# Performance work log

Hardware: AMD Instinct MI355X
Metric: run time of the kernel (lower is better)

## Reference

```python
import jax, jax.numpy as jnp
import numpy as np

DIM = 1024
HEADS = 16
HEAD_DIM = DIM // HEADS
SCALE = HEAD_DIM ** -0.5


def setup_inputs() -> dict:
    key = jax.random.key(0)
    k1, k2, k3 = jax.random.split(key, 3)
    x = jax.random.normal(k1, (4, 2048, DIM), dtype=jnp.float32)
    Wqkv = jax.random.normal(k2, (DIM, 3 * DIM), dtype=jnp.float32) * (DIM ** -0.5)
    Wout = jax.random.normal(k3, (DIM, DIM), dtype=jnp.float32) * (DIM ** -0.5)
    bout = jnp.zeros((DIM,), dtype=jnp.float32)
    return {"x": x, "Wqkv": Wqkv, "Wout": Wout, "bout": bout}


def reference(x, Wqkv, Wout, bout):
    b, n, _ = x.shape
    qkv = x @ Wqkv  # [b, n, 3*dim]
    q, k, v = jnp.split(qkv, 3, axis=-1)
    # [b, n, dim] -> [b, h, n, d]
    def split_heads(t):
        return t.reshape(b, n, HEADS, HEAD_DIM).transpose(0, 2, 1, 3)
    q, k, v = split_heads(q), split_heads(k), split_heads(v)
    dots = jnp.einsum('bhid,bhjd->bhij', q, k) * SCALE
    attn = jax.nn.softmax(dots, axis=-1)
    out = jnp.einsum('bhij,bhjd->bhid', attn, v)
    out = out.transpose(0, 2, 1, 3).reshape(b, n, DIM)
    return out @ Wout + bout  # dropout is identity in eval mode
```

## Files before the change

### kernel.cpp

```cpp
#include <hip/hip_runtime.h>
#include <hip/hip_bf16.h>

#define BATCH 4
#define SEQ   2048
#define DIM   1024
#define HEADS 16
#define HD    64
#define ROWS  (BATCH * SEQ)
#define QKV_N (3 * DIM)
#define ATT_C 0.18033688011f

typedef unsigned short u16;
typedef _Float16 half8 __attribute__((ext_vector_type(8)));
typedef _Float16 half4v __attribute__((ext_vector_type(4)));
typedef float f32x4 __attribute__((ext_vector_type(4)));

__device__ __forceinline__ void gload_lds16(const u16* g, u16* l) {
  typedef const __attribute__((address_space(1))) unsigned int* gp_t;
  typedef __attribute__((address_space(3))) unsigned int* lp_t;
  __builtin_amdgcn_global_load_lds((gp_t)(const void*)g, (lp_t)(void*)l, 16, 0, 0);
}

__global__ __launch_bounds__(256) void conv_x(const float* __restrict__ x,
                                              u16* __restrict__ xh) {
  int i = blockIdx.x * 256 + threadIdx.x;
  float4 v = ((const float4*)x)[i];
  half4v h = {(_Float16)v.x, (_Float16)v.y, (_Float16)v.z, (_Float16)v.w};
  *(half4v*)&xh[(size_t)i * 4] = h;
}

__global__ __launch_bounds__(256) void conv_w(const float* __restrict__ W,
                                              u16* __restrict__ Wt,
                                              int K, int N) {
  __shared__ float T[64][65];
  const int tid = threadIdx.x;
  const int k0 = blockIdx.y * 64, n0 = blockIdx.x * 64;
#pragma unroll
  for (int j = 0; j < 4; ++j) {
    int k = j * 16 + (tid >> 4), n4 = (tid & 15) * 4;
    float4 v = *(const float4*)(W + (size_t)(k0 + k) * N + n0 + n4);
    T[k][n4 + 0] = v.x; T[k][n4 + 1] = v.y; T[k][n4 + 2] = v.z; T[k][n4 + 3] = v.w;
  }
  __syncthreads();
#pragma unroll
  for (int j = 0; j < 4; ++j) {
    int n = j * 16 + (tid >> 4), k4 = (tid & 15) * 4;
    half4v w = {(_Float16)T[k4 + 0][n], (_Float16)T[k4 + 1][n],
                (_Float16)T[k4 + 2][n], (_Float16)T[k4 + 3][n]};
    *(half4v*)&Wt[(size_t)(n0 + n) * K + k0 + k4] = w;
  }
}

template <int MODE>
__global__ __launch_bounds__(256) void gemm_bt(
    const u16* __restrict__ A, const u16* __restrict__ Bt,
    const float* __restrict__ bias, void* __restrict__ Cv,
    u16* __restrict__ Qg, u16* __restrict__ Kg, u16* __restrict__ VtG,
    int M, int N, int K) {
  __shared__ u16 As[128 * 32];
  __shared__ u16 Bs[128 * 32];

  const int tid = threadIdx.x;
  const int wave = tid >> 6, lane = tid & 63;
  const int q4 = lane >> 4, c = lane & 15;
  const int wm = wave >> 1, wn = wave & 1;
  const int row0 = blockIdx.y * 128, col0 = blockIdx.x * 128;
  const int rr = lane >> 2, seg = lane & 3;

  f32x4 acc[4][4];
#pragma unroll
  for (int mi = 0; mi < 4; ++mi)
#pragma unroll
    for (int ni = 0; ni < 4; ++ni) acc[mi][ni] = (f32x4){0.f, 0.f, 0.f, 0.f};

  for (int k0 = 0; k0 < K; k0 += 32) {
#pragma unroll
    for (int i = 0; i < 2; ++i) {
      int chunk = wave * 2 + i;
      gload_lds16(A + (size_t)(row0 + chunk * 16 + rr) * K + k0 + seg * 8,
                  &As[chunk * 512]);
      gload_lds16(Bt + (size_t)(col0 + chunk * 16 + rr) * K + k0 + seg * 8,
                  &Bs[chunk * 512]);
    }
    __syncthreads();

    half8 af[4], bf[4];
#pragma unroll
    for (int mi = 0; mi < 4; ++mi)
      af[mi] = *(const half8*)&As[(wm * 64 + mi * 16 + c) * 32 + q4 * 8];
#pragma unroll
    for (int ni = 0; ni < 4; ++ni)
      bf[ni] = *(const half8*)&Bs[(wn * 64 + ni * 16 + c) * 32 + q4 * 8];
#pragma unroll
    for (int mi = 0; mi < 4; ++mi)
#pragma unroll
      for (int ni = 0; ni < 4; ++ni)
        acc[mi][ni] = __builtin_amdgcn_mfma_f32_16x16x32_f16(
            af[mi], bf[ni], acc[mi][ni], 0, 0, 0);
    __syncthreads();
  }

#pragma unroll
  for (int mi = 0; mi < 4; ++mi)
#pragma unroll
    for (int ni = 0; ni < 4; ++ni) {
      int colg = col0 + wn * 64 + ni * 16 + c;
      if (MODE == 0) {
        float bv = bias[colg];
#pragma unroll
        for (int r = 0; r < 4; ++r) {
          int rowg = row0 + wm * 64 + mi * 16 + q4 * 4 + r;
          ((float*)Cv)[(size_t)rowg * N + colg] = acc[mi][ni][r] + bv;
        }
      } else {
        int rowg0 = row0 + wm * 64 + mi * 16 + q4 * 4;
        int b  = rowg0 >> 11;
        int which = colg >> 10;
        int rem = colg & 1023;
        int hh = rem >> 6, d = rem & 63;
        size_t bh = (size_t)(b * HEADS + hh);
        if (which == 2) {
          int i0 = rowg0 & 2047;
          half4v pv = {(_Float16)acc[mi][ni][0], (_Float16)acc[mi][ni][1],
                       (_Float16)acc[mi][ni][2], (_Float16)acc[mi][ni][3]};
          *(half4v*)&VtG[(bh * HD + d) * SEQ + i0] = pv;
        } else {
          u16* dst = (which == 0) ? Qg : Kg;
          float sc = (which == 0) ? ATT_C : 1.0f;
#pragma unroll
          for (int r = 0; r < 4; ++r) {
            int i = (rowg0 + r) & 2047;
            ((_Float16*)dst)[(bh * SEQ + i) * HD + d] =
                (_Float16)(acc[mi][ni][r] * sc);
          }
        }
      }
    }
}

__global__ __launch_bounds__(256, 3) void attn_mfma(
    const u16* __restrict__ Qg, const u16* __restrict__ Kg,
    const u16* __restrict__ VtG, u16* __restrict__ ctx) {
  const int L  = blockIdx.x;
  const int bh = L & 63;
  const int b  = bh >> 4, h = bh & 15;
  const int qt = L >> 6;

  __shared__ u16 Ks[2][64 * 32];
  __shared__ u16 Vt[2][64 * 32];
  __shared__ u16 Ps[128 * 72];
  __shared__ float lred[4][128];
  __shared__ float lfull[128];

  const int tid  = threadIdx.x;
  const int wave = tid >> 6;
  const int lane = tid & 63;
  const int q4   = lane >> 4;
  const int c    = lane & 15;
  const int rr   = lane >> 2, seg = lane & 3;
  const int sseg = seg ^ (rr & 3);
  const int rsw  = (c & 3);

  const size_t bhb = (size_t)bh;
  const int qrow0 = qt * 128;

  half8 qf[8][2];
#pragma unroll
  for (int nt = 0; nt < 8; ++nt)
#pragma unroll
    for (int half = 0; half < 2; ++half)
      qf[nt][half] = *(const half8*)&Qg[(bhb * SEQ + qrow0 + nt * 16 + c) * HD
                                        + half * 32 + q4 * 8];

  f32x4 o_acc[2][4];
#pragma unroll
  for (int sub = 0; sub < 2; ++sub)
#pragma unroll
    for (int dt = 0; dt < 4; ++dt) o_acc[sub][dt] = (f32x4){0.f, 0.f, 0.f, 0.f};
  float lp[8] = {0.f, 0.f, 0.f, 0.f, 0.f, 0.f, 0.f, 0.f};

  for (int j0 = 0; j0 < SEQ; j0 += 64) {
    __syncthreads();
#pragma unroll
    for (int half = 0; half < 2; ++half) {
      gload_lds16(Kg + (bhb * SEQ + j0 + wave * 16 + rr) * HD
                      + half * 32 + sseg * 8,
                  &Ks[half][wave * 16 * 32]);
      gload_lds16(VtG + (bhb * HD + wave * 16 + rr) * SEQ + j0
                      + half * 32 + sseg * 8,
                  &Vt[half][wave * 16 * 32]);
    }
    __syncthreads();

    half8 af0 = *(const half8*)&Ks[0][(wave * 16 + c) * 32 + (q4 ^ rsw) * 8];
    half8 af1 = *(const half8*)&Ks[1][(wave * 16 + c) * 32 + (q4 ^ rsw) * 8];
#pragma unroll
    for (int nt = 0; nt < 8; ++nt) {
      f32x4 st = (f32x4){0.f, 0.f, 0.f, 0.f};
      st = __builtin_amdgcn_mfma_f32_16x16x32_f16(af0, qf[nt][0], st, 0, 0, 0);
      st = __builtin_amdgcn_mfma_f32_16x16x32_f16(af1, qf[nt][1], st, 0, 0, 0);
      float p0 = __builtin_amdgcn_exp2f(st[0]);
      float p1 = __builtin_amdgcn_exp2f(st[1]);
      float p2 = __builtin_amdgcn_exp2f(st[2]);
      float p3 = __builtin_amdgcn_exp2f(st[3]);
      lp[nt] += (p0 + p1) + (p2 + p3);
      half4v w = {(_Float16)p0, (_Float16)p1, (_Float16)p2, (_Float16)p3};
      *(half4v*)&Ps[(nt * 16 + c) * 72 + wave * 16 + q4 * 4] = w;
    }
    __syncthreads();

    half8 vb0[4], vb1[4];
#pragma unroll
    for (int dt = 0; dt < 4; ++dt) {
      vb0[dt] = *(const half8*)&Vt[0][(dt * 16 + c) * 32 + (q4 ^ rsw) * 8];
      vb1[dt] = *(const half8*)&Vt[1][(dt * 16 + c) * 32 + (q4 ^ rsw) * 8];
    }
#pragma unroll
    for (int sub = 0; sub < 2; ++sub) {
      half8 pa0 = *(const half8*)&Ps[(wave * 32 + sub * 16 + c) * 72 + q4 * 8];
      half8 pa1 = *(const half8*)&Ps[(wave * 32 + sub * 16 + c) * 72 + 32 + q4 * 8];
#pragma unroll
      for (int dt = 0; dt < 4; ++dt) {
        o_acc[sub][dt] = __builtin_amdgcn_mfma_f32_16x16x32_f16(
            pa0, vb0[dt], o_acc[sub][dt], 0, 0, 0);
        o_acc[sub][dt] = __builtin_amdgcn_mfma_f32_16x16x32_f16(
            pa1, vb1[dt], o_acc[sub][dt], 0, 0, 0);
      }
    }
  }

#pragma unroll
  for (int nt = 0; nt < 8; ++nt) {
    lp[nt] += __shfl_xor(lp[nt], 16);
    lp[nt] += __shfl_xor(lp[nt], 32);
  }
  if (q4 == 0)
#pragma unroll
    for (int nt = 0; nt < 8; ++nt) lred[wave][nt * 16 + c] = lp[nt];
  __syncthreads();
  if (tid < 128)
    lfull[tid] = lred[0][tid] + lred[1][tid] + lred[2][tid] + lred[3][tid];
  __syncthreads();

#pragma unroll
  for (int sub = 0; sub < 2; ++sub)
#pragma unroll
    for (int r = 0; r < 4; ++r) {
      int i = wave * 32 + sub * 16 + q4 * 4 + r;
      float inv = 1.0f / lfull[i];
      size_t row = (size_t)b * SEQ + qrow0 + i;
#pragma unroll
      for (int dt = 0; dt < 4; ++dt)
        ((_Float16*)ctx)[row * DIM + h * HD + dt * 16 + c] =
            (_Float16)(o_acc[sub][dt][r] * inv);
    }
}

extern "C" void kernel_launch(void* const* d_in, const int* in_sizes, int n_in,
                              void* d_out, int out_size, void* d_ws, size_t ws_size,
                              hipStream_t stream) {
  const float* x    = (const float*)d_in[0];
  const float* Wqkv = (const float*)d_in[1];
  const float* Wout = (const float*)d_in[2];
  const float* bout = (const float*)d_in[3];
  float* out = (float*)d_out;

  u16* xh   = (u16*)d_ws;
  u16* Wqt  = xh  + (size_t)ROWS * DIM;
  u16* Wot  = Wqt + (size_t)QKV_N * DIM;
  u16* Qg   = Wot + (size_t)DIM * DIM;
  u16* Kg   = Qg  + (size_t)BATCH * HEADS * SEQ * HD;
  u16* VtG  = Kg  + (size_t)BATCH * HEADS * SEQ * HD;
  u16* ctxh = VtG + (size_t)BATCH * HEADS * HD * SEQ;

  conv_x<<<ROWS * DIM / 4 / 256, 256, 0, stream>>>(x, xh);
  conv_w<<<dim3(QKV_N / 64, DIM / 64), 256, 0, stream>>>(Wqkv, Wqt, DIM, QKV_N);
  conv_w<<<dim3(DIM / 64, DIM / 64), 256, 0, stream>>>(Wout, Wot, DIM, DIM);

  gemm_bt<1><<<dim3(QKV_N / 128, ROWS / 128), 256, 0, stream>>>(
      xh, Wqt, nullptr, nullptr, Qg, Kg, VtG, ROWS, QKV_N, DIM);

  attn_mfma<<<dim3(1024), 256, 0, stream>>>(Qg, Kg, VtG, ctxh);

  gemm_bt<0><<<dim3(DIM / 128, ROWS / 128), 256, 0, stream>>>(
      ctxh, Wot, bout, out, nullptr, nullptr, nullptr, ROWS, DIM, DIM);
}
```

Baseline: 313.2 us.

## Double-buffer K/V LDS tiles in attention kernel to prefetch next block

Splits the K and V LDS tiles into two buffers. The next 64-key tile is issued via global_load_lds at the start of each iteration, while the current tile is consumed from the other buffer. This drops the leading barrier pair per iteration in favour of one trailing barrier, aiming to hide global load latency behind the QK^T and softmax work. The cost is twice the LDS for K/V. The existing mid-loop barrier may force an early wait on the outstanding loads, which would limit how much overlap is gained.

```diff
diff --git a/kernel.cpp b/kernel.cpp
--- a/kernel.cpp
+++ b/kernel.cpp
@@ -146,8 +146,8 @@
   const int b  = bh >> 4, h = bh & 15;
   const int qt = L >> 6;
 
-  __shared__ u16 Ks[2][64 * 32];
-  __shared__ u16 Vt[2][64 * 32];
+  __shared__ u16 Ks[2][2][64 * 32];
+  __shared__ u16 Vt[2][2][64 * 32];
   __shared__ u16 Ps[128 * 72];
   __shared__ float lred[4][128];
   __shared__ float lfull[128];
@@ -164,6 +164,14 @@
   const size_t bhb = (size_t)bh;
   const int qrow0 = qt * 128;
 
+#pragma unroll
+  for (int half = 0; half < 2; ++half) {
+    gload_lds16(Kg + (bhb * SEQ + wave * 16 + rr) * HD + half * 32 + sseg * 8,
+                &Ks[0][half][wave * 16 * 32]);
+    gload_lds16(VtG + (bhb * HD + wave * 16 + rr) * SEQ + half * 32 + sseg * 8,
+                &Vt[0][half][wave * 16 * 32]);
+  }
+
   half8 qf[8][2];
 #pragma unroll
   for (int nt = 0; nt < 8; ++nt)
@@ -179,21 +187,26 @@
     for (int dt = 0; dt < 4; ++dt) o_acc[sub][dt] = (f32x4){0.f, 0.f, 0.f, 0.f};
   float lp[8] = {0.f, 0.f, 0.f, 0.f, 0.f, 0.f, 0.f, 0.f};
 
+  __syncthreads();
+
   for (int j0 = 0; j0 < SEQ; j0 += 64) {
-    __syncthreads();
-#pragma unroll
-    for (int half = 0; half < 2; ++half) {
-      gload_lds16(Kg + (bhb * SEQ + j0 + wave * 16 + rr) * HD
-                      + half * 32 + sseg * 8,
-                  &Ks[half][wave * 16 * 32]);
-      gload_lds16(VtG + (bhb * HD + wave * 16 + rr) * SEQ + j0
-                      + half * 32 + sseg * 8,
-                  &Vt[half][wave * 16 * 32]);
-    }
-    __syncthreads();
-
-    half8 af0 = *(const half8*)&Ks[0][(wave * 16 + c) * 32 + (q4 ^ rsw) * 8];
-    half8 af1 = *(const half8*)&Ks[1][(wave * 16 + c) * 32 + (q4 ^ rsw) * 8];
+    const int cb = (j0 >> 6) & 1;
+
+    if (j0 + 64 < SEQ) {
+      const int jn = j0 + 64, nb = cb ^ 1;
+#pragma unroll
+      for (int half = 0; half < 2; ++half) {
+        gload_lds16(Kg + (bhb * SEQ + jn + wave * 16 + rr) * HD
+                        + half * 32 + sseg * 8,
+                    &Ks[nb][half][wave * 16 * 32]);
+        gload_lds16(VtG + (bhb * HD + wave * 16 + rr) * SEQ + jn
+                        + half * 32 + sseg * 8,
+                    &Vt[nb][half][wave * 16 * 32]);
+      }
+    }
+
+    half8 af0 = *(const half8*)&Ks[cb][0][(wave * 16 + c) * 32 + (q4 ^ rsw) * 8];
+    half8 af1 = *(const half8*)&Ks[cb][1][(wave * 16 + c) * 32 + (q4 ^ rsw) * 8];
 #pragma unroll
     for (int nt = 0; nt < 8; ++nt) {
       f32x4 st = (f32x4){0.f, 0.f, 0.f, 0.f};
@@ -212,8 +225,8 @@
     half8 vb0[4], vb1[4];
 #pragma unroll
     for (int dt = 0; dt < 4; ++dt) {
-      vb0[dt] = *(const half8*)&Vt[0][(dt * 16 + c) * 32 + (q4 ^ rsw) * 8];
-      vb1[dt] = *(const half8*)&Vt[1][(dt * 16 + c) * 32 + (q4 ^ rsw) * 8];
+      vb0[dt] = *(const half8*)&Vt[cb][0][(dt * 16 + c) * 32 + (q4 ^ rsw) * 8];
+      vb1[dt] = *(const half8*)&Vt[cb][1][(dt * 16 + c) * 32 + (q4 ^ rsw) * 8];
     }
 #pragma unroll
     for (int sub = 0; sub < 2; ++sub) {
@@ -227,6 +240,7 @@
             pa1, vb1[dt], o_acc[sub][dt], 0, 0, 0);
       }
     }
+    __syncthreads();
   }
 
 #pragma unroll
```

Result: faster. 305.8 us (-2.4%).

## Use 8-wave attention blocks over 128-key tiles with per-wave 16-row outputs

Applied to the files above, without the earlier changes.

The attention kernel now runs 512 threads (8 waves) per block and processes 128 keys per iteration instead of 64. Each wave computes QK^T for 16 keys and then P·V for 16 query rows, instead of 32 rows as before. This halves the number of loop iterations and barriers, and cuts the accumulator registers per wave so more waves can be resident. The cost is a larger LDS footprint for K, V and P, and V fragments are now reloaded from LDS inside the inner loop rather than held in registers.

```diff
diff --git a/kernel.cpp b/kernel.cpp
--- a/kernel.cpp
+++ b/kernel.cpp
@@ -138,7 +138,9 @@
     }
 }
 
-__global__ __launch_bounds__(256, 3) void attn_mfma(
+#define PSTR 140
+
+__global__ __launch_bounds__(512, 4) void attn_mfma(
     const u16* __restrict__ Qg, const u16* __restrict__ Kg,
     const u16* __restrict__ VtG, u16* __restrict__ ctx) {
   const int L  = blockIdx.x;
@@ -146,10 +148,10 @@
   const int b  = bh >> 4, h = bh & 15;
   const int qt = L >> 6;
 
-  __shared__ u16 Ks[2][64 * 32];
-  __shared__ u16 Vt[2][64 * 32];
-  __shared__ u16 Ps[128 * 72];
-  __shared__ float lred[4][128];
+  __shared__ u16 Ks[2][128 * 32];
+  __shared__ u16 Vt[4][64 * 32];
+  __shared__ u16 Ps[128 * PSTR];
+  __shared__ float lred[8][128];
   __shared__ float lfull[128];
 
   const int tid  = threadIdx.x;
@@ -168,27 +170,27 @@
 #pragma unroll
   for (int nt = 0; nt < 8; ++nt)
 #pragma unroll
-    for (int half = 0; half < 2; ++half)
-      qf[nt][half] = *(const half8*)&Qg[(bhb * SEQ + qrow0 + nt * 16 + c) * HD
-                                        + half * 32 + q4 * 8];
-
-  f32x4 o_acc[2][4];
-#pragma unroll
-  for (int sub = 0; sub < 2; ++sub)
-#pragma unroll
-    for (int dt = 0; dt < 4; ++dt) o_acc[sub][dt] = (f32x4){0.f, 0.f, 0.f, 0.f};
+    for (int kh = 0; kh < 2; ++kh)
+      qf[nt][kh] = *(const half8*)&Qg[(bhb * SEQ + qrow0 + nt * 16 + c) * HD
+                                      + kh * 32 + q4 * 8];
+
+  f32x4 o_acc[4];
+#pragma unroll
+  for (int dt = 0; dt < 4; ++dt) o_acc[dt] = (f32x4){0.f, 0.f, 0.f, 0.f};
   float lp[8] = {0.f, 0.f, 0.f, 0.f, 0.f, 0.f, 0.f, 0.f};
 
-  for (int j0 = 0; j0 < SEQ; j0 += 64) {
-    __syncthreads();
-#pragma unroll
-    for (int half = 0; half < 2; ++half) {
-      gload_lds16(Kg + (bhb * SEQ + j0 + wave * 16 + rr) * HD
-                      + half * 32 + sseg * 8,
-                  &Ks[half][wave * 16 * 32]);
-      gload_lds16(VtG + (bhb * HD + wave * 16 + rr) * SEQ + j0
-                      + half * 32 + sseg * 8,
-                  &Vt[half][wave * 16 * 32]);
+  for (int j0 = 0; j0 < SEQ; j0 += 128) {
+    __syncthreads();
+
+#pragma unroll
+    for (int i = 0; i < 2; ++i) {
+      int chunk = wave * 2 + i;
+      int kh = chunk >> 3, jr = chunk & 7;
+      gload_lds16(Kg + (bhb * SEQ + j0 + jr * 16 + rr) * HD + kh * 32 + sseg * 8,
+                  &Ks[kh][jr * 16 * 32]);
+      int q = chunk >> 2, d16 = chunk & 3;
+      gload_lds16(VtG + (bhb * HD + d16 * 16 + rr) * SEQ + j0 + q * 32 + sseg * 8,
+                  &Vt[q][d16 * 16 * 32]);
     }
     __syncthreads();
 
@@ -205,26 +207,18 @@
       float p3 = __builtin_amdgcn_exp2f(st[3]);
       lp[nt] += (p0 + p1) + (p2 + p3);
       half4v w = {(_Float16)p0, (_Float16)p1, (_Float16)p2, (_Float16)p3};
-      *(half4v*)&Ps[(nt * 16 + c) * 72 + wave * 16 + q4 * 4] = w;
-    }
-    __syncthreads();
-
-    half8 vb0[4], vb1[4];
-#pragma unroll
-    for (int dt = 0; dt < 4; ++dt) {
-      vb0[dt] = *(const half8*)&Vt[0][(dt * 16 + c) * 32 + (q4 ^ rsw) * 8];
-      vb1[dt] = *(const half8*)&Vt[1][(dt * 16 + c) * 32 + (q4 ^ rsw) * 8];
-    }
-#pragma unroll
-    for (int sub = 0; sub < 2; ++sub) {
-      half8 pa0 = *(const half8*)&Ps[(wave * 32 + sub * 16 + c) * 72 + q4 * 8];
-      half8 pa1 = *(const half8*)&Ps[(wave * 32 + sub * 16 + c) * 72 + 32 + q4 * 8];
+      *(half4v*)&Ps[(nt * 16 + c) * PSTR + wave * 16 + q4 * 4] = w;
+    }
+    __syncthreads();
+
+#pragma unroll
+    for (int kc = 0; kc < 4; ++kc) {
+      half8 pa = *(const half8*)&Ps[(wave * 16 + c) * PSTR + kc * 32 + q4 * 8];
 #pragma unroll
       for (int dt = 0; dt < 4; ++dt) {
-        o_acc[sub][dt] = __builtin_amdgcn_mfma_f32_16x16x32_f16(
-            pa0, vb0[dt], o_acc[sub][dt], 0, 0, 0);
-        o_acc[sub][dt] = __builtin_amdgcn_mfma_f32_16x16x32_f16(
-            pa1, vb1[dt], o_acc[sub][dt], 0, 0, 0);
+        half8 vb = *(const half8*)&Vt[kc][(dt * 16 + c) * 32 + (q4 ^ rsw) * 8];
+        o_acc[dt] = __builtin_amdgcn_mfma_f32_16x16x32_f16(
+            pa, vb, o_acc[dt], 0, 0, 0);
       }
     }
   }
@@ -238,22 +232,24 @@
 #pragma unroll
     for (int nt = 0; nt < 8; ++nt) lred[wave][nt * 16 + c] = lp[nt];
   __syncthreads();
-  if (tid < 128)
-    lfull[tid] = lred[0][tid] + lred[1][tid] + lred[2][tid] + lred[3][tid];
+  if (tid < 128) {
+    float s = 0.f;
+#pragma unroll
+    for (int w = 0; w < 8; ++w) s += lred[w][tid];
+    lfull[tid] = s;
+  }
   __syncthreads();
 
 #pragma unroll
-  for (int sub = 0; sub < 2; ++sub)
-#pragma unroll
-    for (int r = 0; r < 4; ++r) {
-      int i = wave * 32 + sub * 16 + q4 * 4 + r;
-      float inv = 1.0f / lfull[i];
-      size_t row = (size_t)b * SEQ + qrow0 + i;
-#pragma unroll
-      for (int dt = 0; dt < 4; ++dt)
-        ((_Float16*)ctx)[row * DIM + h * HD + dt * 16 + c] =
-            (_Float16)(o_acc[sub][dt][r] * inv);
-    }
+  for (int r = 0; r < 4; ++r) {
+    int i = wave * 16 + q4 * 4 + r;
+    float inv = 1.0f / lfull[i];
+    size_t row = (size_t)b * SEQ + qrow0 + i;
+#pragma unroll
+    for (int dt = 0; dt < 4; ++dt)
+      ((_Float16*)ctx)[row * DIM + h * HD + dt * 16 + c] =
+          (_Float16)(o_acc[dt][r] * inv);
+  }
 }
 
 extern "C" void kernel_launch(void* const* d_in, const int* in_sizes, int n_in,
@@ -280,7 +276,7 @@
   gemm_bt<1><<<dim3(QKV_N / 128, ROWS / 128), 256, 0, stream>>>(
       xh, Wqt, nullptr, nullptr, Qg, Kg, VtG, ROWS, QKV_N, DIM);
 
-  attn_mfma<<<dim3(1024), 256, 0, stream>>>(Qg, Kg, VtG, ctxh);
+  attn_mfma<<<dim3(1024), 512, 0, stream>>>(Qg, Kg, VtG, ctxh);
 
   gemm_bt<0><<<dim3(DIM / 128, ROWS / 128), 256, 0, stream>>>(
       ctxh, Wot, bout, out, nullptr, nullptr, nullptr, ROWS, DIM, DIM);
```

Result: faster. 296.2 us (-5.4%).
